# Optimization experiments

Measured on AMD Instinct MI355X. Metric: run time of the kernel, lower is better.

## Reference

```python
import jax, jax.numpy as jnp
import numpy as np

# Static config (matches init_kwargs)
B, H, W, C = 16, 56, 56, 512
WS, SHIFT, NH = 7, 3, 16
HD = C // NH
N = WS * WS
NW = (H // WS) * (W // WS)
SCALE = HD ** -0.5
EPS = 1e-5


def _relative_position_index():
    coords = np.stack(np.meshgrid(np.arange(WS), np.arange(WS), indexing='ij'))  # (2,WS,WS)
    flat = coords.reshape(2, -1)                       # (2,N)
    rel = flat[:, :, None] - flat[:, None, :]          # (2,N,N)
    rel = rel.transpose(1, 2, 0).astype(np.int64)
    rel[..., 0] += WS - 1
    rel[..., 1] += WS - 1
    rel[..., 0] *= 2 * WS - 1
    return rel.sum(-1)                                 # (N,N)


def _window_partition_np(x):
    # x: (H,W) numpy -> (NW, N)
    return x.reshape(H // WS, WS, W // WS, WS).transpose(0, 2, 1, 3).reshape(-1, N)


def _attn_mask():
    img = np.zeros((H, W))
    cnt = 0
    for hs in (slice(0, -WS), slice(-WS, -SHIFT), slice(-SHIFT, None)):
        for ws_ in (slice(0, -WS), slice(-WS, -SHIFT), slice(-SHIFT, None)):
            img[hs, ws_] = cnt
            cnt += 1
    mw = _window_partition_np(img)                     # (NW, N)
    diff = mw[:, None, :] - mw[:, :, None]             # (NW, N, N)
    return np.where(diff != 0, -100.0, 0.0).astype(np.float32)


REL_IDX = jnp.asarray(_relative_position_index())
ATTN_MASK = jnp.asarray(_attn_mask())


def window_partition(x):
    # x: (B,H,W,C) -> (B*NW, N, C)
    x = x.reshape(B, H // WS, WS, W // WS, WS, C)
    return x.transpose(0, 1, 3, 2, 4, 5).reshape(-1, N, C)


def window_reverse(w):
    # w: (B*NW, N, C) -> (B,H,W,C)
    x = w.reshape(B, H // WS, W // WS, WS, WS, C)
    return x.transpose(0, 1, 3, 2, 4, 5).reshape(B, H, W, C)


def layer_norm(x, g, b):
    m = x.mean(-1, keepdims=True)
    v = jnp.mean((x - m) ** 2, axis=-1, keepdims=True)
    return (x - m) * jax.lax.rsqrt(v + EPS) * g + b


def before_cross_attention(x, g, b):
    # x: (B, L, C) -> shifted windows (B*NW, N, C)
    x = layer_norm(x, g, b).reshape(B, H, W, C)
    x = jnp.roll(x, (-SHIFT, -SHIFT), axis=(1, 2))
    return window_partition(x)


def get_qkv(x, Wqkv, bqkv):
    # x: (B_, N, C); Wqkv: (C, 3C)
    qkv = (x @ Wqkv + bqkv).reshape(-1, N, 3, NH, HD).transpose(2, 0, 3, 1, 4)
    return qkv[0], qkv[1], qkv[2]  # each (B_, NH, N, HD)


def setup_inputs() -> dict:
    key = jax.random.key(0)
    ks = jax.random.split(key, 10)
    s = 0.02
    return {
        'rescaled': jax.random.normal(ks[0], (B, H * W, C), jnp.float32),
        'rescaler': jax.random.normal(ks[1], (B, H * W, C), jnp.float32),
        'gamma_a': jnp.ones((C,), jnp.float32),
        'beta_a': jnp.zeros((C,), jnp.float32),
        'gamma_b': jnp.ones((C,), jnp.float32),
        'beta_b': jnp.zeros((C,), jnp.float32),
        'Wqkv_a': jax.random.normal(ks[2], (C, 3 * C), jnp.float32) * s,
        'bqkv_a': jnp.zeros((3 * C,), jnp.float32),
        'Wqkv_b': jax.random.normal(ks[3], (C, 3 * C), jnp.float32) * s,
        'bqkv_b': jnp.zeros((3 * C,), jnp.float32),
        'rpb_table': jax.random.normal(ks[4], ((2 * WS - 1) ** 2, NH), jnp.float32) * s,
        'Wproj': jax.random.normal(ks[5], (C, C), jnp.float32) * s,
        'bproj': jnp.zeros((C,), jnp.float32),
    }


def reference(rescaled, rescaler, gamma_a, beta_a, gamma_b, beta_b,
              Wqkv_a, bqkv_a, Wqkv_b, bqkv_b, rpb_table, Wproj, bproj):
    # norm + shift + window partition for both streams
    xw = before_cross_attention(rescaled, gamma_a, beta_a)   # (B*NW, N, C)
    yw = before_cross_attention(rescaler, gamma_b, beta_b)

    q_a, k_a, v_a = get_qkv(xw, Wqkv_a, bqkv_a)  # rescaled stream
    q_b, k_b, v_b = get_qkv(yw, Wqkv_b, bqkv_b)  # rescaler stream
    # same_key_query=False: q from rescaler, k & v from rescaled
    q, k, v = q_b * SCALE, k_a, v_a

    attn = jnp.einsum('bhnd,bhmd->bhnm', q, k)               # (B*NW, NH, N, N)
    rpb = rpb_table[REL_IDX.reshape(-1)].reshape(N, N, NH).transpose(2, 0, 1)
    attn = attn + rpb[None]
    attn = attn.reshape(B, NW, NH, N, N) + ATTN_MASK[None, :, None]
    attn = jax.nn.softmax(attn.reshape(-1, NH, N, N), axis=-1)

    out = jnp.einsum('bhnm,bhmd->bhnd', attn, v)             # (B*NW, NH, N, HD)
    out = out.transpose(0, 2, 1, 3).reshape(-1, N, C)
    out = out @ Wproj + bproj

    # window reverse + un-shift, back to (B, L, C)
    x = window_reverse(out)
    x = jnp.roll(x, (SHIFT, SHIFT), axis=(1, 2))
    return x.reshape(B, H * W, C)
```

## Files before the change

kernel.cpp:

```cpp
#include <hip/hip_runtime.h>
#include <hip/hip_bf16.h>


typedef short bf16x8 __attribute__((ext_vector_type(8)));
typedef float f32x4 __attribute__((ext_vector_type(4)));
typedef unsigned short u16;

#define MTOT 50176
#define SCALE_ 0.17677669529663687f

__device__ __forceinline__ u16 f2bf(float f) {
    __hip_bfloat16 h = __float2bfloat16(f);
    return *reinterpret_cast<u16*>(&h);
}
__device__ __forceinline__ float bf2f(u16 u) {
    union { unsigned int i; float f; } t; t.i = ((unsigned int)u) << 16; return t.f;
}

#define ASYNC_COPY16(g, l)                                                      \
    __builtin_amdgcn_global_load_lds((__attribute__((address_space(1))) void*)(g), \
                                     (__attribute__((address_space(3))) void*)(l), 16, 0, 0)

__global__ __launch_bounds__(256) void wconv_kernel(
    const float* __restrict__ Wqkv_a, const float* __restrict__ Wqkv_b,
    const float* __restrict__ Wproj, u16* __restrict__ Wt)
{
    const int idx = blockIdx.x * 256 + threadIdx.x;
    const int r = idx >> 9;
    const int k = idx & 511;
    float val;
    if (r < 512)       val = Wqkv_b[k * 1536 + r];
    else if (r < 1536) val = Wqkv_a[k * 1536 + r];
    else               val = Wproj[k * 512 + (r - 1536)];
    Wt[idx] = f2bf(val);
}

__global__ __launch_bounds__(256) void build_bias_kernel(
    const float* __restrict__ rpb, float* __restrict__ bias)
{
    const int blk = blockIdx.x;
    const int mid = blk >> 4, head = blk & 15;
    const int whq = (mid >> 1) & 1, wwq = mid & 1;
    for (int t = threadIdx.x; t < 4096; t += 256) {
        const int i = t >> 6, j = t & 63;
        float v;
        if (i < 49 && j < 49) {
            const int ih = i / 7, iw = i - ih * 7;
            const int jh = j / 7, jw = j - jh * 7;
            v = rpb[((ih - jh + 6) * 13 + (iw - jw + 6)) * 16 + head];
            const int li = (whq ? (ih < 4 ? 1 : 2) : 0) * 3 + (wwq ? (iw < 4 ? 1 : 2) : 0);
            const int lj = (whq ? (jh < 4 ? 1 : 2) : 0) * 3 + (wwq ? (jw < 4 ? 1 : 2) : 0);
            if (li != lj) v -= 100.0f;
        } else {
            v = -3.0e38f;
        }
        bias[(size_t)blk * 4096 + t] = v;
    }
}

__device__ __forceinline__ void ln_one(
    const float* __restrict__ src, const float* __restrict__ g,
    const float* __restrict__ bt, u16* __restrict__ dst, int lane)
{
    const float4 v0 = *(const float4*)(src + lane * 8);
    const float4 v1 = *(const float4*)(src + lane * 8 + 4);
    float s = v0.x + v0.y + v0.z + v0.w + v1.x + v1.y + v1.z + v1.w;
    float q = v0.x*v0.x + v0.y*v0.y + v0.z*v0.z + v0.w*v0.w
            + v1.x*v1.x + v1.y*v1.y + v1.z*v1.z + v1.w*v1.w;
#pragma unroll
    for (int o = 32; o >= 1; o >>= 1) { s += __shfl_xor(s, o); q += __shfl_xor(q, o); }
    const float mean = s * (1.0f / 512.0f);
    const float rstd = rsqrtf(q * (1.0f / 512.0f) - mean * mean + 1e-5f);
    const float4 g0 = *(const float4*)(g + lane * 8);
    const float4 g1 = *(const float4*)(g + lane * 8 + 4);
    const float4 b0 = *(const float4*)(bt + lane * 8);
    const float4 b1 = *(const float4*)(bt + lane * 8 + 4);
    u16 o8[8];
    o8[0] = f2bf((v0.x - mean) * rstd * g0.x + b0.x);
    o8[1] = f2bf((v0.y - mean) * rstd * g0.y + b0.y);
    o8[2] = f2bf((v0.z - mean) * rstd * g0.z + b0.z);
    o8[3] = f2bf((v0.w - mean) * rstd * g0.w + b0.w);
    o8[4] = f2bf((v1.x - mean) * rstd * g1.x + b1.x);
    o8[5] = f2bf((v1.y - mean) * rstd * g1.y + b1.y);
    o8[6] = f2bf((v1.z - mean) * rstd * g1.z + b1.z);
    o8[7] = f2bf((v1.w - mean) * rstd * g1.w + b1.w);
    int4 pk;
    pk.x = (int)(((unsigned)o8[1] << 16) | o8[0]);
    pk.y = (int)(((unsigned)o8[3] << 16) | o8[2]);
    pk.z = (int)(((unsigned)o8[5] << 16) | o8[4]);
    pk.w = (int)(((unsigned)o8[7] << 16) | o8[6]);
    *(int4*)(dst + lane * 8) = pk;
}

__global__ __launch_bounds__(256) void ln_window_kernel(
    const float* __restrict__ xa, const float* __restrict__ xb,
    const float* __restrict__ ga, const float* __restrict__ bea,
    const float* __restrict__ gb, const float* __restrict__ beb,
    u16* __restrict__ xw, u16* __restrict__ yw)
{
    const int wave = threadIdx.x >> 6, lane = threadIdx.x & 63;
    const int row = blockIdx.x * 4 + wave;
    const int win = row / 49, n = row - win * 49;
    const int b = win >> 6, wi = win & 63;
    const int wh = wi >> 3, ww = wi & 7;
    const int ih = n / 7, iw = n - ih * 7;
    int h = wh * 7 + ih + 3; if (h >= 56) h -= 56;
    int w = ww * 7 + iw + 3; if (w >= 56) w -= 56;
    const size_t src = ((size_t)b * 3136 + (size_t)h * 56 + w) * 512;
    const size_t dst = (size_t)row * 512;
    ln_one(xa + src, ga, bea, xw + dst, lane);
    ln_one(xb + src, gb, beb, yw + dst, lane);
}

#define GEMM_PROLOG()                                                           \
    __shared__ __align__(16) u16 As[128 * 64];                                  \
    __shared__ __align__(16) u16 Bs[128 * 64];                                  \
    const int tid = threadIdx.x;                                                \
    const int lane = tid & 63;                                                  \
    const int wv = tid >> 6;                                                    \
    const int wr = wv >> 1, wc = wv & 1;                                        \
    const int rowl = lane & 15, kg = lane >> 4;                                 \
    f32x4 acc[4][4];                                                            \
    for (int i = 0; i < 4; ++i)                                                 \
        for (int j = 0; j < 4; ++j)                                             \
            acc[i][j] = (f32x4){0.f, 0.f, 0.f, 0.f};                            \
    const int sr = tid >> 3;                                                    \
    const int scc = (tid & 7) * 8;                                              \
    const u16* Ab = Asrc + (size_t)(mt * 128 + sr) * 512 + scc;                 \
    const u16* Bb = Bsrc + (size_t)sr * 512 + scc;                              \
    char* AsDst = (char*)As + tid * 16;                                         \
    char* BsDst = (char*)Bs + tid * 16;                                         \
    for (int kt = 0; kt < 8; ++kt) {                                            \
        const int k0 = kt * 64;                                                 \
        _Pragma("unroll")                                                       \
        for (int i = 0; i < 4; ++i) {                                           \
            ASYNC_COPY16(Ab + (size_t)i * 32 * 512 + k0, AsDst + i * 4096);     \
            ASYNC_COPY16(Bb + (size_t)i * 32 * 512 + k0, BsDst + i * 4096);     \
        }                                                                       \
        asm volatile("s_waitcnt vmcnt(0)" ::: "memory");                        \
        __syncthreads();                                                        \
        _Pragma("unroll")                                                       \
        for (int kk = 0; kk < 64; kk += 32) {                                   \
            bf16x8 af[4], bfr[4];                                               \
            _Pragma("unroll")                                                   \
            for (int i = 0; i < 4; ++i)                                         \
                af[i] = *(const bf16x8*)(As + (wr * 64 + i * 16 + rowl) * 64 + kk + kg * 8); \
            _Pragma("unroll")                                                   \
            for (int j = 0; j < 4; ++j)                                         \
                bfr[j] = *(const bf16x8*)(Bs + (wc * 64 + j * 16 + rowl) * 64 + kk + kg * 8); \
            _Pragma("unroll")                                                   \
            for (int i = 0; i < 4; ++i) {                                       \
                _Pragma("unroll")                                               \
                for (int j = 0; j < 4; ++j)                                     \
                    acc[i][j] = __builtin_amdgcn_mfma_f32_16x16x32_bf16(        \
                        af[i], bfr[j], acc[i][j], 0, 0, 0);                     \
            }                                                                   \
        }                                                                       \
        __syncthreads();                                                        \
    }

__global__ __launch_bounds__(256) void gemm_qkv_kernel(
    const u16* __restrict__ xw, const u16* __restrict__ yw,
    const u16* __restrict__ Wt,
    const float* __restrict__ bqkv_a, const float* __restrict__ bqkv_b,
    u16* __restrict__ qb, u16* __restrict__ kb, u16* __restrict__ vb)
{
    const int bid = blockIdx.x;
    const int swz = (bid & 7) * 588 + (bid >> 3);
    const int nt = swz % 12;
    const int mt = swz / 12;
    const u16* Asrc = (nt < 4) ? yw : xw;
    const u16* Bsrc = Wt + (size_t)(nt * 128) * 512;
    GEMM_PROLOG()

#pragma unroll
    for (int j = 0; j < 4; ++j) {
        const int col = nt * 128 + wc * 64 + j * 16 + rowl;
        const bool isq = (col < 512);
        const float bias_ = isq ? bqkv_b[col] : bqkv_a[col];
        u16* dst = isq ? qb : (col < 1024 ? kb : vb);
        const int pcol = col & 511;
#pragma unroll
        for (int i = 0; i < 4; ++i) {
#pragma unroll
            for (int r = 0; r < 4; ++r) {
                const int row = mt * 128 + wr * 64 + i * 16 + kg * 4 + r;
                float val = acc[i][j][r] + bias_;
                if (isq) val *= SCALE_;
                dst[(size_t)row * 512 + pcol] = f2bf(val);
            }
        }
    }
}

__global__ __launch_bounds__(256) void gemm_proj_kernel(
    const u16* __restrict__ attn_out, const u16* __restrict__ WtProj,
    const float* __restrict__ bproj, float* __restrict__ out)
{
    const int bid = blockIdx.x;
    const int swz = (bid & 7) * 196 + (bid >> 3);
    const int nt = swz & 3;
    const int mt = swz >> 2;
    const u16* Asrc = attn_out;
    const u16* Bsrc = WtProj + (size_t)(nt * 128) * 512;
    GEMM_PROLOG()

#pragma unroll
    for (int j = 0; j < 4; ++j) {
        const int col = nt * 128 + wc * 64 + j * 16 + rowl;
        const float bias_ = bproj[col];
#pragma unroll
        for (int i = 0; i < 4; ++i) {
#pragma unroll
            for (int r = 0; r < 4; ++r) {
                const int row = mt * 128 + wr * 64 + i * 16 + kg * 4 + r;
                const int win = row / 49;
                const int nw = row - win * 49;
                const int b = win >> 6, wi = win & 63;
                const int wh = wi >> 3, ww = wi & 7;
                const int ih = nw / 7, iw = nw - ih * 7;
                int h = wh * 7 + ih + 3; if (h >= 56) h -= 56;
                int w = ww * 7 + iw + 3; if (w >= 56) w -= 56;
                out[((size_t)b * 3136 + (size_t)h * 56 + w) * 512 + col] =
                    acc[i][j][r] + bias_;
            }
        }
    }
}

__global__ __launch_bounds__(256) void attn_kernel(
    const u16* __restrict__ qb, const u16* __restrict__ kb,
    const u16* __restrict__ vb, const float* __restrict__ bias,
    u16* __restrict__ attn_out)
{
    __shared__ __align__(16) u16 VT[32 * 64];
    __shared__ __align__(16) u16 P[64 * 64];
    const int tid = threadIdx.x;
    const int wh_id = blockIdx.x;
    const int win = wh_id >> 4, head = wh_id & 15;
    const int lane = tid & 63, wvi = tid >> 6;
    const int rowl = lane & 15, kg = lane >> 4;
    const size_t base = (size_t)win * 49 * 512 + head * 32;

    {
        const int j = tid >> 2, d0 = (tid & 3) * 8;
        const bf16x8 v8 = *(const bf16x8*)(vb + base + (size_t)j * 512 + d0);
        const int cj = j >> 3, je = j & 7;
#pragma unroll
        for (int m = 0; m < 8; ++m) {
            const int d = d0 + m;
            VT[d * 64 + ((cj ^ (d & 7)) * 8) + je] = (u16)v8[m];
        }
    }

    const bf16x8 aq = *(const bf16x8*)(qb + base + (size_t)(wvi * 16 + rowl) * 512 + kg * 8);
    f32x4 accS[4];
#pragma unroll
    for (int j = 0; j < 4; ++j) {
        const bf16x8 bk = *(const bf16x8*)(kb + base + (size_t)(j * 16 + rowl) * 512 + kg * 8);
        accS[j] = __builtin_amdgcn_mfma_f32_16x16x32_bf16(
            aq, bk, (f32x4){0.f, 0.f, 0.f, 0.f}, 0, 0, 0);
    }

    const int wi = win & 63;
    const int mid = (((wi >> 3) == 7) ? 2 : 0) + (((wi & 7) == 7) ? 1 : 0);
    const float* bptr = bias + ((size_t)(mid * 16 + head) << 12);
#pragma unroll
    for (int j = 0; j < 4; ++j)
#pragma unroll
        for (int r = 0; r < 4; ++r)
            accS[j][r] += bptr[(wvi * 16 + kg * 4 + r) * 64 + j * 16 + rowl];

    float rinv[4];
#pragma unroll
    for (int r = 0; r < 4; ++r) {
        float m = fmaxf(fmaxf(accS[0][r], accS[1][r]), fmaxf(accS[2][r], accS[3][r]));
#pragma unroll
        for (int o = 1; o <= 8; o <<= 1) m = fmaxf(m, __shfl_xor(m, o));
        float s = 0.f;
#pragma unroll
        for (int j = 0; j < 4; ++j) {
            accS[j][r] = __expf(accS[j][r] - m);
            s += accS[j][r];
        }
#pragma unroll
        for (int o = 1; o <= 8; o <<= 1) s += __shfl_xor(s, o);
        rinv[r] = __frcp_rn(s);
    }

#pragma unroll
    for (int j = 0; j < 4; ++j) {
        const int c = j * 2 + (rowl >> 3);
#pragma unroll
        for (int r = 0; r < 4; ++r) {
            const int row = wvi * 16 + kg * 4 + r;
            P[row * 64 + ((c ^ (row & 7)) * 8) + (rowl & 7)] = f2bf(accS[j][r]);
        }
    }

    __syncthreads();

    f32x4 accO[2];
#pragma unroll
    for (int dt = 0; dt < 2; ++dt) {
        accO[dt] = (f32x4){0.f, 0.f, 0.f, 0.f};
#pragma unroll
        for (int kb_ = 0; kb_ < 2; ++kb_) {
            const int prow = wvi * 16 + rowl;
            const int ca = kb_ * 4 + kg;
            const bf16x8 ap = *(const bf16x8*)(P + prow * 64 + ((ca ^ (prow & 7)) * 8));
            const int vd = dt * 16 + rowl;
            const bf16x8 bv = *(const bf16x8*)(VT + vd * 64 + ((ca ^ (vd & 7)) * 8));
            accO[dt] = __builtin_amdgcn_mfma_f32_16x16x32_bf16(ap, bv, accO[dt], 0, 0, 0);
        }
    }

#pragma unroll
    for (int dt = 0; dt < 2; ++dt) {
#pragma unroll
        for (int r = 0; r < 4; ++r) {
            const int i = wvi * 16 + kg * 4 + r;
            if (i < 49)
                attn_out[base + (size_t)i * 512 + dt * 16 + rowl] =
                    f2bf(accO[dt][r] * rinv[r]);
        }
    }
}

extern "C" void kernel_launch(void* const* d_in, const int* in_sizes, int n_in,
                              void* d_out, int out_size, void* d_ws, size_t ws_size,
                              hipStream_t stream) {
    (void)in_sizes; (void)n_in; (void)out_size; (void)ws_size;
    const float* rescaled = (const float*)d_in[0];
    const float* rescaler = (const float*)d_in[1];
    const float* gamma_a  = (const float*)d_in[2];
    const float* beta_a   = (const float*)d_in[3];
    const float* gamma_b  = (const float*)d_in[4];
    const float* beta_b   = (const float*)d_in[5];
    const float* Wqkv_a   = (const float*)d_in[6];
    const float* bqkv_a   = (const float*)d_in[7];
    const float* Wqkv_b   = (const float*)d_in[8];
    const float* bqkv_b   = (const float*)d_in[9];
    const float* rpb      = (const float*)d_in[10];
    const float* Wproj    = (const float*)d_in[11];
    const float* bproj    = (const float*)d_in[12];
    float* out = (float*)d_out;

    char* ws = (char*)d_ws;
    const size_t SZ = (size_t)MTOT * 512 * 2;
    u16* xw = (u16*)ws;
    u16* yw = (u16*)(ws + SZ);
    u16* qb = (u16*)(ws + 2 * SZ);
    u16* kb = (u16*)(ws + 3 * SZ);
    u16* vb = (u16*)(ws + 4 * SZ);
    u16* Wt = (u16*)(ws + 5 * SZ);
    float* bias = (float*)(ws + 5 * SZ + 2097152);
    u16* attn_out = xw;

    wconv_kernel<<<4096, 256, 0, stream>>>(Wqkv_a, Wqkv_b, Wproj, Wt);
    build_bias_kernel<<<64, 256, 0, stream>>>(rpb, bias);
    ln_window_kernel<<<MTOT / 4, 256, 0, stream>>>(
        rescaled, rescaler, gamma_a, beta_a, gamma_b, beta_b, xw, yw);
    gemm_qkv_kernel<<<4704, 256, 0, stream>>>(
        xw, yw, Wt, bqkv_a, bqkv_b, qb, kb, vb);
    attn_kernel<<<16384, 256, 0, stream>>>(qb, kb, vb, bias, attn_out);
    gemm_proj_kernel<<<1568, 256, 0, stream>>>(
        attn_out, Wt + (size_t)1536 * 512, bproj, out);
}
```

Measured before the change: 578.1 us.

## Widen GEMM tiles to 128x256 with 8 waves and XOR-swizzled LDS

```diff
diff --git a/kernel.cpp b/kernel.cpp
--- a/kernel.cpp
+++ b/kernel.cpp
@@ -112,42 +112,46 @@
     ln_one(xb + src, gb, beb, yw + dst, lane);
 }
 
-#define GEMM_PROLOG()                                                           \
+#define GEMM8_MAIN()                                                            \
     __shared__ __align__(16) u16 As[128 * 64];                                  \
-    __shared__ __align__(16) u16 Bs[128 * 64];                                  \
+    __shared__ __align__(16) u16 Bs[256 * 64];                                  \
     const int tid = threadIdx.x;                                                \
     const int lane = tid & 63;                                                  \
     const int wv = tid >> 6;                                                    \
-    const int wr = wv >> 1, wc = wv & 1;                                        \
+    const int wm = wv >> 2, wn = wv & 3;                                        \
     const int rowl = lane & 15, kg = lane >> 4;                                 \
+    const int sw = rowl & 7;                                                    \
     f32x4 acc[4][4];                                                            \
     for (int i = 0; i < 4; ++i)                                                 \
         for (int j = 0; j < 4; ++j)                                             \
             acc[i][j] = (f32x4){0.f, 0.f, 0.f, 0.f};                            \
-    const int sr = tid >> 3;                                                    \
-    const int scc = (tid & 7) * 8;                                              \
-    const u16* Ab = Asrc + (size_t)(mt * 128 + sr) * 512 + scc;                 \
-    const u16* Bb = Bsrc + (size_t)sr * 512 + scc;                              \
-    char* AsDst = (char*)As + tid * 16;                                         \
-    char* BsDst = (char*)Bs + tid * 16;                                         \
+    const int srow = tid >> 3;                                                  \
+    const int clog = (tid & 7) ^ (srow & 7);                                    \
+    const u16* Ab = Asrc + (size_t)(mt * 128 + srow) * 512 + clog * 8;          \
+    const u16* Bb = Bsrc + (size_t)srow * 512 + clog * 8;                       \
+    char* AsD = (char*)As + tid * 16;                                           \
+    char* BsD = (char*)Bs + tid * 16;                                           \
     for (int kt = 0; kt < 8; ++kt) {                                            \
         const int k0 = kt * 64;                                                 \
         _Pragma("unroll")                                                       \
-        for (int i = 0; i < 4; ++i) {                                           \
-            ASYNC_COPY16(Ab + (size_t)i * 32 * 512 + k0, AsDst + i * 4096);     \
-            ASYNC_COPY16(Bb + (size_t)i * 32 * 512 + k0, BsDst + i * 4096);     \
-        }                                                                       \
+        for (int r = 0; r < 2; ++r)                                             \
+            ASYNC_COPY16(Ab + (size_t)r * 64 * 512 + k0, AsD + r * 8192);       \
+        _Pragma("unroll")                                                       \
+        for (int r = 0; r < 4; ++r)                                             \
+            ASYNC_COPY16(Bb + (size_t)r * 64 * 512 + k0, BsD + r * 8192);       \
         asm volatile("s_waitcnt vmcnt(0)" ::: "memory");                        \
         __syncthreads();                                                        \
         _Pragma("unroll")                                                       \
-        for (int kk = 0; kk < 64; kk += 32) {                                   \
+        for (int kk = 0; kk < 2; ++kk) {                                        \
+            const int kch = kg + kk * 4;                                        \
+            const int sco = (kch ^ sw) * 8;                                     \
             bf16x8 af[4], bfr[4];                                               \
             _Pragma("unroll")                                                   \
             for (int i = 0; i < 4; ++i)                                         \
-                af[i] = *(const bf16x8*)(As + (wr * 64 + i * 16 + rowl) * 64 + kk + kg * 8); \
+                af[i] = *(const bf16x8*)(As + (wm * 64 + i * 16 + rowl) * 64 + sco); \
             _Pragma("unroll")                                                   \
             for (int j = 0; j < 4; ++j)                                         \
-                bfr[j] = *(const bf16x8*)(Bs + (wc * 64 + j * 16 + rowl) * 64 + kk + kg * 8); \
+                bfr[j] = *(const bf16x8*)(Bs + (wn * 64 + j * 16 + rowl) * 64 + sco); \
             _Pragma("unroll")                                                   \
             for (int i = 0; i < 4; ++i) {                                       \
                 _Pragma("unroll")                                               \
@@ -159,33 +163,35 @@
         __syncthreads();                                                        \
     }
 
-__global__ __launch_bounds__(256) void gemm_qkv_kernel(
+__global__ __launch_bounds__(512) void gemm_qkv_kernel(
     const u16* __restrict__ xw, const u16* __restrict__ yw,
     const u16* __restrict__ Wt,
     const float* __restrict__ bqkv_a, const float* __restrict__ bqkv_b,
     u16* __restrict__ qb, u16* __restrict__ kb, u16* __restrict__ vb)
 {
     const int bid = blockIdx.x;
-    const int swz = (bid & 7) * 588 + (bid >> 3);
-    const int nt = swz % 12;
-    const int mt = swz / 12;
-    const u16* Asrc = (nt < 4) ? yw : xw;
-    const u16* Bsrc = Wt + (size_t)(nt * 128) * 512;
-    GEMM_PROLOG()
-
+    const int swz = (bid & 7) * 294 + (bid >> 3);
+    const int nt = swz % 6;
+    const int mt = swz / 6;
+    const u16* Asrc = (nt < 2) ? yw : xw;
+    const u16* Bsrc = Wt + (size_t)(nt * 256) * 512;
+    GEMM8_MAIN()
+
+    u16* dst; const float* bvec; bool isq = false;
+    if (nt < 2)      { dst = qb; bvec = bqkv_b; isq = true; }
+    else if (nt < 4) { dst = kb; bvec = bqkv_a; }
+    else             { dst = vb; bvec = bqkv_a; }
 #pragma unroll
     for (int j = 0; j < 4; ++j) {
-        const int col = nt * 128 + wc * 64 + j * 16 + rowl;
-        const bool isq = (col < 512);
-        const float bias_ = isq ? bqkv_b[col] : bqkv_a[col];
-        u16* dst = isq ? qb : (col < 1024 ? kb : vb);
+        const int col = nt * 256 + wn * 64 + j * 16 + rowl;
+        const float bias_ = bvec[col];
         const int pcol = col & 511;
 #pragma unroll
         for (int i = 0; i < 4; ++i) {
 #pragma unroll
-            for (int r = 0; r < 4; ++r) {
-                const int row = mt * 128 + wr * 64 + i * 16 + kg * 4 + r;
-                float val = acc[i][j][r] + bias_;
+            for (int rr = 0; rr < 4; ++rr) {
+                const int row = mt * 128 + wm * 64 + i * 16 + kg * 4 + rr;
+                float val = acc[i][j][rr] + bias_;
                 if (isq) val *= SCALE_;
                 dst[(size_t)row * 512 + pcol] = f2bf(val);
             }
@@ -193,27 +199,27 @@
     }
 }
 
-__global__ __launch_bounds__(256) void gemm_proj_kernel(
+__global__ __launch_bounds__(512) void gemm_proj_kernel(
     const u16* __restrict__ attn_out, const u16* __restrict__ WtProj,
     const float* __restrict__ bproj, float* __restrict__ out)
 {
     const int bid = blockIdx.x;
-    const int swz = (bid & 7) * 196 + (bid >> 3);
-    const int nt = swz & 3;
-    const int mt = swz >> 2;
+    const int swz = (bid & 7) * 98 + (bid >> 3);
+    const int nt = swz & 1;
+    const int mt = swz >> 1;
     const u16* Asrc = attn_out;
-    const u16* Bsrc = WtProj + (size_t)(nt * 128) * 512;
-    GEMM_PROLOG()
+    const u16* Bsrc = WtProj + (size_t)(nt * 256) * 512;
+    GEMM8_MAIN()
 
 #pragma unroll
     for (int j = 0; j < 4; ++j) {
-        const int col = nt * 128 + wc * 64 + j * 16 + rowl;
+        const int col = nt * 256 + wn * 64 + j * 16 + rowl;
         const float bias_ = bproj[col];
 #pragma unroll
         for (int i = 0; i < 4; ++i) {
 #pragma unroll
-            for (int r = 0; r < 4; ++r) {
-                const int row = mt * 128 + wr * 64 + i * 16 + kg * 4 + r;
+            for (int rr = 0; rr < 4; ++rr) {
+                const int row = mt * 128 + wm * 64 + i * 16 + kg * 4 + rr;
                 const int win = row / 49;
                 const int nw = row - win * 49;
                 const int b = win >> 6, wi = win & 63;
@@ -222,7 +228,7 @@
                 int h = wh * 7 + ih + 3; if (h >= 56) h -= 56;
                 int w = ww * 7 + iw + 3; if (w >= 56) w -= 56;
                 out[((size_t)b * 3136 + (size_t)h * 56 + w) * 512 + col] =
-                    acc[i][j][r] + bias_;
+                    acc[i][j][rr] + bias_;
             }
         }
     }
@@ -361,9 +367,9 @@
     build_bias_kernel<<<64, 256, 0, stream>>>(rpb, bias);
     ln_window_kernel<<<MTOT / 4, 256, 0, stream>>>(
         rescaled, rescaler, gamma_a, beta_a, gamma_b, beta_b, xw, yw);
-    gemm_qkv_kernel<<<4704, 256, 0, stream>>>(
+    gemm_qkv_kernel<<<2352, 512, 0, stream>>>(
         xw, yw, Wt, bqkv_a, bqkv_b, qb, kb, vb);
     attn_kernel<<<16384, 256, 0, stream>>>(qb, kb, vb, bias, attn_out);
-    gemm_proj_kernel<<<1568, 256, 0, stream>>>(
+    gemm_proj_kernel<<<784, 512, 0, stream>>>(
         attn_out, Wt + (size_t)1536 * 512, bproj, out);
 }
```

After: 521.1 us. 9.9% less time.
